# Performance work log

Measured on AMD Instinct MI355X. Metric: run time of the kernel, lower is better.

The kernel has to match this reference:

```python
import jax, jax.numpy as jnp
import numpy as np

E, I, O = 8, 1024, 1024   # num_experts, in_features, out_features
B = 16                    # number of molecular systems (segments)
N = 16384                 # total rows (atoms * coeffs); sum(mole_sizes) == N


def setup_inputs() -> dict:
    key = jax.random.key(0)
    k1, k2, k3, k4 = jax.random.split(key, 4)
    scale = (1.0 / I) ** 0.5
    x = jax.random.normal(k1, (N, I), dtype=jnp.float32)
    # init_linear: uniform(-k, k) with k = sqrt(1/in_features)
    weights = scale * 2.0 * (jax.random.uniform(k2, (E, O, I), dtype=jnp.float32) - 0.5)
    bias = scale * 2.0 * (jax.random.uniform(k3, (O,), dtype=jnp.float32) - 0.5)
    expert_mixing_coefficients = jax.random.uniform(k4, (B, E), dtype=jnp.float32)
    # segment sizes per system; equal sizes summing exactly to N (static under jit)
    mole_sizes = jnp.full((B,), N // B, dtype=jnp.int32)
    return {
        "x": x,
        "weights": weights,
        "bias": bias,
        "expert_mixing_coefficients": expert_mixing_coefficients,
        "mole_sizes": mole_sizes,
    }


def reference(x, weights, bias, expert_mixing_coefficients, mole_sizes):
    # Original: W_b = einsum('eoi,be->bio', weights, coeff); then segment_mm
    # applies x_seg_b @ W_b for each row-segment b.  By linearity this equals
    # projecting x through each expert and mixing with per-row coefficients,
    # which avoids materializing [B, I, O] synthesized weights per segment
    # while computing identical math.
    n = x.shape[0]
    b = expert_mixing_coefficients.shape[0]
    seg_id = jnp.repeat(jnp.arange(b), mole_sizes, total_repeat_length=n)  # [N]
    ct = expert_mixing_coefficients[seg_id]                               # [N, E]
    proj = jnp.einsum('ni,eoi->neo', x, weights)                          # [N, E, O]
    y = jnp.einsum('neo,ne->no', proj, ct) + bias                         # [N, O]
    return y
```

## Files before the change

### kernel.cpp

```cpp
#include <hip/hip_runtime.h>
#include <hip/hip_bf16.h>
#include <stdint.h>

constexpr int E_NUM  = 8;
constexpr int I_DIM  = 1024;
constexpr int O_DIM  = 1024;
constexpr int B_SEG  = 16;
constexpr int N_ROWS = 16384;

constexpr int BM = 128, BN = 128, BK = 32;

typedef __bf16 bf16x8 __attribute__((ext_vector_type(8)));
typedef float  f32x4  __attribute__((ext_vector_type(4)));
typedef unsigned short ushortx4 __attribute__((ext_vector_type(4)));

__device__ __forceinline__ unsigned short f2bf(float f) {
    unsigned int u = __float_as_uint(f);
    u += 0x7fffu + ((u >> 16) & 1u);
    return (unsigned short)(u >> 16);
}

__global__ __launch_bounds__(256) void cvt_x(const float* __restrict__ x,
                                             unsigned short* __restrict__ xb) {
    const size_t S = (size_t)4096 * 256;
    size_t i = (size_t)blockIdx.x * 256 + threadIdx.x;
    const float4* x4 = (const float4*)x;
    ushortx4* o4 = (ushortx4*)xb;
    float4 v0 = x4[i], v1 = x4[i + S], v2 = x4[i + 2 * S], v3 = x4[i + 3 * S];
    ushortx4 a, b, c, d;
    a[0] = f2bf(v0.x); a[1] = f2bf(v0.y); a[2] = f2bf(v0.z); a[3] = f2bf(v0.w);
    b[0] = f2bf(v1.x); b[1] = f2bf(v1.y); b[2] = f2bf(v1.z); b[3] = f2bf(v1.w);
    c[0] = f2bf(v2.x); c[1] = f2bf(v2.y); c[2] = f2bf(v2.z); c[3] = f2bf(v2.w);
    d[0] = f2bf(v3.x); d[1] = f2bf(v3.y); d[2] = f2bf(v3.z); d[3] = f2bf(v3.w);
    o4[i]         = a;
    o4[i + S]     = b;
    o4[i + 2 * S] = c;
    o4[i + 3 * S] = d;
}

__global__ __launch_bounds__(256) void synth_w(const float* __restrict__ w,
                                               const float* __restrict__ coeff,
                                               unsigned short* __restrict__ wb) {
    __shared__ float sc[B_SEG * E_NUM];
    const int tid = threadIdx.x;
    if (tid < B_SEG * E_NUM) sc[tid] = coeff[tid];
    __syncthreads();

    const size_t nvec = (size_t)O_DIM * I_DIM / 4;
    const size_t i = (size_t)blockIdx.x * 256 + tid;
    const float4* w4 = (const float4*)w;
    ushortx4* wb4 = (ushortx4*)wb;

    float4 wv[E_NUM];
#pragma unroll
    for (int e = 0; e < E_NUM; e++)
        wv[e] = w4[(size_t)e * nvec + i];

#pragma unroll
    for (int b = 0; b < B_SEG; b++) {
        float a0 = 0.f, a1 = 0.f, a2 = 0.f, a3 = 0.f;
#pragma unroll
        for (int e = 0; e < E_NUM; e++) {
            float c = sc[b * E_NUM + e];
            a0 += c * wv[e].x; a1 += c * wv[e].y;
            a2 += c * wv[e].z; a3 += c * wv[e].w;
        }
        ushortx4 o;
        o[0] = f2bf(a0); o[1] = f2bf(a1); o[2] = f2bf(a2); o[3] = f2bf(a3);
        wb4[(size_t)b * nvec + i] = o;
    }
}

__global__ __launch_bounds__(256) void gemm_moe(
    const unsigned short* __restrict__ xb,
    const unsigned short* __restrict__ wb,
    const float* __restrict__ bias,
    const int* __restrict__ msz,
    float* __restrict__ out)
{
    __shared__ __align__(16) unsigned short sA[BM * BK];
    __shared__ __align__(16) unsigned short sB[BN * BK];

    const int lid  = blockIdx.x;
    const int xcd  = lid & 7;
    const int idx  = lid >> 3;
    const int seg  = (xcd << 1) | (idx >> 6);
    const int s    = idx & 63;
    const int mloc = s >> 3;
    const int nblk = s & 7;

    int off = 0;
    for (int b = 0; b < seg; b++) off += msz[b];
    const int row0 = off + mloc * BM;
    const int col0 = nblk * BN;
    const unsigned short* wseg = wb + (size_t)seg * O_DIM * I_DIM;

    const int tid  = threadIdx.x;
    const int wave = tid >> 6;
    const int lane = tid & 63;
    const int wm = wave >> 1, wn = wave & 1;
    const int quad = lane >> 4, l16 = lane & 15;

    const int srow   = wave * 32 + (lane >> 2);
    const int schunk = (lane & 3) ^ ((lane >> 3) & 3);
    const int scol   = schunk * 8;

    const unsigned short* gA = xb   + (size_t)(row0 + srow) * I_DIM + scol;
    const unsigned short* gB = wseg + (size_t)(col0 + srow) * I_DIM + scol;
    const int ldsOfs0 = (wave * 32) * BK;
    const int ldsOfs1 = (wave * 32 + 16) * BK;

    const int rchunk = (quad ^ ((l16 >> 1) & 3)) * 8;

    f32x4 acc[4][4];
#pragma unroll
    for (int m = 0; m < 4; m++)
#pragma unroll
        for (int n = 0; n < 4; n++)
            acc[m][n] = (f32x4){0.f, 0.f, 0.f, 0.f};

#pragma unroll 1
    for (int k0 = 0; k0 < I_DIM; k0 += BK) {
        __builtin_amdgcn_global_load_lds(
            (const __attribute__((address_space(1))) void*)(gA + k0),
            (__attribute__((address_space(3))) void*)(&sA[ldsOfs0]), 16, 0, 0);
        __builtin_amdgcn_global_load_lds(
            (const __attribute__((address_space(1))) void*)(gA + 16 * I_DIM + k0),
            (__attribute__((address_space(3))) void*)(&sA[ldsOfs1]), 16, 0, 0);
        __builtin_amdgcn_global_load_lds(
            (const __attribute__((address_space(1))) void*)(gB + k0),
            (__attribute__((address_space(3))) void*)(&sB[ldsOfs0]), 16, 0, 0);
        __builtin_amdgcn_global_load_lds(
            (const __attribute__((address_space(1))) void*)(gB + 16 * I_DIM + k0),
            (__attribute__((address_space(3))) void*)(&sB[ldsOfs1]), 16, 0, 0);
        __syncthreads();

        bf16x8 af[4], bfr[4];
#pragma unroll
        for (int m = 0; m < 4; m++)
            af[m] = *(const bf16x8*)&sA[(wm * 64 + m * 16 + l16) * BK + rchunk];
#pragma unroll
        for (int n = 0; n < 4; n++)
            bfr[n] = *(const bf16x8*)&sB[(wn * 64 + n * 16 + l16) * BK + rchunk];

#pragma unroll
        for (int m = 0; m < 4; m++)
#pragma unroll
            for (int n = 0; n < 4; n++)
                acc[m][n] = __builtin_amdgcn_mfma_f32_16x16x32_bf16(
                    af[m], bfr[n], acc[m][n], 0, 0, 0);

        __syncthreads();
    }

    float bv[4];
#pragma unroll
    for (int n = 0; n < 4; n++)
        bv[n] = bias[col0 + wn * 64 + n * 16 + l16];

#pragma unroll
    for (int m = 0; m < 4; m++) {
#pragma unroll
        for (int r = 0; r < 4; r++) {
            int row = row0 + wm * 64 + m * 16 + quad * 4 + r;
            float* po = out + (size_t)row * O_DIM + col0 + wn * 64 + l16;
#pragma unroll
            for (int n = 0; n < 4; n++)
                po[n * 16] = acc[m][n][r] + bv[n];
        }
    }
}

extern "C" void kernel_launch(void* const* d_in, const int* in_sizes, int n_in,
                              void* d_out, int out_size, void* d_ws, size_t ws_size,
                              hipStream_t stream) {
    const float* x     = (const float*)d_in[0];
    const float* w     = (const float*)d_in[1];
    const float* bias  = (const float*)d_in[2];
    const float* coeff = (const float*)d_in[3];
    const int*   msz   = (const int*)d_in[4];
    float* out = (float*)d_out;

    unsigned short* xb = (unsigned short*)d_ws;
    unsigned short* wb = xb + (size_t)N_ROWS * I_DIM;

    cvt_x<<<4096, 256, 0, stream>>>(x, xb);
    synth_w<<<1024, 256, 0, stream>>>(w, coeff, wb);
    gemm_moe<<<1024, 256, 0, stream>>>(xb, wb, bias, msz, out);
}
```

Baseline: 214.2 us.

## Fuse fp32-to-bf16 conversion of x into GEMM with register-staged double buffering

```diff
diff --git a/kernel.cpp b/kernel.cpp
--- a/kernel.cpp
+++ b/kernel.cpp
@@ -9,8 +9,11 @@
 constexpr int N_ROWS = 16384;
 
 constexpr int BM = 128, BN = 128, BK = 32;
+constexpr int KITERS = I_DIM / BK;
+constexpr int TILE_ELEMS = BM * BK;
 
 typedef __bf16 bf16x8 __attribute__((ext_vector_type(8)));
+typedef __bf16 bf16x4 __attribute__((ext_vector_type(4)));
 typedef float  f32x4  __attribute__((ext_vector_type(4)));
 typedef unsigned short ushortx4 __attribute__((ext_vector_type(4)));
 
@@ -18,24 +21,6 @@
     unsigned int u = __float_as_uint(f);
     u += 0x7fffu + ((u >> 16) & 1u);
     return (unsigned short)(u >> 16);
-}
-
-__global__ __launch_bounds__(256) void cvt_x(const float* __restrict__ x,
-                                             unsigned short* __restrict__ xb) {
-    const size_t S = (size_t)4096 * 256;
-    size_t i = (size_t)blockIdx.x * 256 + threadIdx.x;
-    const float4* x4 = (const float4*)x;
-    ushortx4* o4 = (ushortx4*)xb;
-    float4 v0 = x4[i], v1 = x4[i + S], v2 = x4[i + 2 * S], v3 = x4[i + 3 * S];
-    ushortx4 a, b, c, d;
-    a[0] = f2bf(v0.x); a[1] = f2bf(v0.y); a[2] = f2bf(v0.z); a[3] = f2bf(v0.w);
-    b[0] = f2bf(v1.x); b[1] = f2bf(v1.y); b[2] = f2bf(v1.z); b[3] = f2bf(v1.w);
-    c[0] = f2bf(v2.x); c[1] = f2bf(v2.y); c[2] = f2bf(v2.z); c[3] = f2bf(v2.w);
-    d[0] = f2bf(v3.x); d[1] = f2bf(v3.y); d[2] = f2bf(v3.z); d[3] = f2bf(v3.w);
-    o4[i]         = a;
-    o4[i + S]     = b;
-    o4[i + 2 * S] = c;
-    o4[i + 3 * S] = d;
 }
 
 __global__ __launch_bounds__(256) void synth_w(const float* __restrict__ w,
@@ -72,14 +57,14 @@
 }
 
 __global__ __launch_bounds__(256) void gemm_moe(
-    const unsigned short* __restrict__ xb,
+    const float* __restrict__ x,
     const unsigned short* __restrict__ wb,
     const float* __restrict__ bias,
     const int* __restrict__ msz,
     float* __restrict__ out)
 {
-    __shared__ __align__(16) unsigned short sA[BM * BK];
-    __shared__ __align__(16) unsigned short sB[BN * BK];
+    __shared__ __align__(16) unsigned short sA[2 * TILE_ELEMS];
+    __shared__ __align__(16) unsigned short sB[2 * TILE_ELEMS];
 
     const int lid  = blockIdx.x;
     const int xcd  = lid & 7;
@@ -101,16 +86,26 @@
     const int wm = wave >> 1, wn = wave & 1;
     const int quad = lane >> 4, l16 = lane & 15;
 
-    const int srow   = wave * 32 + (lane >> 2);
-    const int schunk = (lane & 3) ^ ((lane >> 3) & 3);
-    const int scol   = schunk * 8;
+    const int arow = tid >> 3;
+    const int apos = tid & 7;
+    const float4* xA = (const float4*)(x + (size_t)(row0 + arow) * I_DIM) + apos;
+    const int aswz = (apos >> 1) ^ ((arow >> 1) & 3);
+    const int offA0 = arow * BK + aswz * 8 + (apos & 1) * 4;
 
-    const unsigned short* gA = xb   + (size_t)(row0 + srow) * I_DIM + scol;
-    const unsigned short* gB = wseg + (size_t)(col0 + srow) * I_DIM + scol;
-    const int ldsOfs0 = (wave * 32) * BK;
-    const int ldsOfs1 = (wave * 32 + 16) * BK;
+    const int brow = tid >> 2;
+    const int bpos = tid & 3;
+    const uint4* wB = (const uint4*)(wseg + (size_t)(col0 + brow) * I_DIM) + bpos;
+    const int bswz = bpos ^ ((brow >> 1) & 3);
+    const int offB0 = brow * BK + bswz * 8;
 
     const int rchunk = (quad ^ ((l16 >> 1) & 3)) * 8;
+    int afOff[4], bfOff[4];
+#pragma unroll
+    for (int m = 0; m < 4; m++)
+        afOff[m] = (wm * 64 + m * 16 + l16) * BK + rchunk;
+#pragma unroll
+    for (int n = 0; n < 4; n++)
+        bfOff[n] = (wn * 64 + n * 16 + l16) * BK + rchunk;
 
     f32x4 acc[4][4];
 #pragma unroll
@@ -119,29 +114,44 @@
         for (int n = 0; n < 4; n++)
             acc[m][n] = (f32x4){0.f, 0.f, 0.f, 0.f};
 
+    float4 aw[4];
+    uint4  bw[2];
+#pragma unroll
+    for (int j = 0; j < 4; j++) aw[j] = xA[j * 8192];
+#pragma unroll
+    for (int j = 0; j < 2; j++) bw[j] = wB[j * 8192];
+
 #pragma unroll 1
-    for (int k0 = 0; k0 < I_DIM; k0 += BK) {
-        __builtin_amdgcn_global_load_lds(
-            (const __attribute__((address_space(1))) void*)(gA + k0),
-            (__attribute__((address_space(3))) void*)(&sA[ldsOfs0]), 16, 0, 0);
-        __builtin_amdgcn_global_load_lds(
-            (const __attribute__((address_space(1))) void*)(gA + 16 * I_DIM + k0),
-            (__attribute__((address_space(3))) void*)(&sA[ldsOfs1]), 16, 0, 0);
-        __builtin_amdgcn_global_load_lds(
-            (const __attribute__((address_space(1))) void*)(gB + k0),
-            (__attribute__((address_space(3))) void*)(&sB[ldsOfs0]), 16, 0, 0);
-        __builtin_amdgcn_global_load_lds(
-            (const __attribute__((address_space(1))) void*)(gB + 16 * I_DIM + k0),
-            (__attribute__((address_space(3))) void*)(&sB[ldsOfs1]), 16, 0, 0);
+    for (int kk = 0; kk < KITERS; ++kk) {
+        const int bufofs = (kk & 1) * TILE_ELEMS;
+
+#pragma unroll
+        for (int j = 0; j < 4; j++) {
+            bf16x4 cv;
+            cv[0] = (__bf16)aw[j].x; cv[1] = (__bf16)aw[j].y;
+            cv[2] = (__bf16)aw[j].z; cv[3] = (__bf16)aw[j].w;
+            *(bf16x4*)&sA[bufofs + offA0 + j * 1024] = cv;
+        }
+#pragma unroll
+        for (int j = 0; j < 2; j++)
+            *(uint4*)&sB[bufofs + offB0 + j * 2048] = bw[j];
+
         __syncthreads();
+
+        if (kk + 1 < KITERS) {
+#pragma unroll
+            for (int j = 0; j < 4; j++) aw[j] = xA[j * 8192 + (kk + 1) * 8];
+#pragma unroll
+            for (int j = 0; j < 2; j++) bw[j] = wB[j * 8192 + (kk + 1) * 4];
+        }
 
         bf16x8 af[4], bfr[4];
 #pragma unroll
         for (int m = 0; m < 4; m++)
-            af[m] = *(const bf16x8*)&sA[(wm * 64 + m * 16 + l16) * BK + rchunk];
+            af[m] = *(const bf16x8*)&sA[bufofs + afOff[m]];
 #pragma unroll
         for (int n = 0; n < 4; n++)
-            bfr[n] = *(const bf16x8*)&sB[(wn * 64 + n * 16 + l16) * BK + rchunk];
+            bfr[n] = *(const bf16x8*)&sB[bufofs + bfOff[n]];
 
 #pragma unroll
         for (int m = 0; m < 4; m++)
@@ -149,8 +159,6 @@
             for (int n = 0; n < 4; n++)
                 acc[m][n] = __builtin_amdgcn_mfma_f32_16x16x32_bf16(
                     af[m], bfr[n], acc[m][n], 0, 0, 0);
-
-        __syncthreads();
     }
 
     float bv[4];
@@ -181,10 +189,8 @@
     const int*   msz   = (const int*)d_in[4];
     float* out = (float*)d_out;
 
-    unsigned short* xb = (unsigned short*)d_ws;
-    unsigned short* wb = xb + (size_t)N_ROWS * I_DIM;
+    unsigned short* wb = (unsigned short*)d_ws;
 
-    cvt_x<<<4096, 256, 0, stream>>>(x, xb);
     synth_w<<<1024, 256, 0, stream>>>(w, coeff, wb);
-    gemm_moe<<<1024, 256, 0, stream>>>(xb, wb, bias, msz, out);
+    gemm_moe<<<1024, 256, 0, stream>>>(x, wb, bias, msz, out);
 }
```

New measurement: 262.9 us. +22.8%, slower.
